# Kernel optimization log

Measured on AMD Instinct MI355X. Metric: run time of the kernel, lower is better.

Reference implementation:

```python
import jax, jax.numpy as jnp
import numpy as np
from jax import lax

# Dimensions
B, D_MODEL, H, W = 2, 128, 96, 96
EXPAND = 2
D_INNER = EXPAND * D_MODEL      # 256
D_STATE = 16
D_CONV = 4
DT_RANK = (D_MODEL + 15) // 16  # 8 (mamba default ceil(d_model/16))


def setup_inputs() -> dict:
    key = jax.random.key(0)
    ks = jax.random.split(key, 16)
    s = 0.02
    return {
        "x": jax.random.normal(ks[0], (B, D_MODEL, H, W), jnp.float32),
        "y": jax.random.normal(ks[1], (B, D_MODEL, H, W), jnp.float32),
        # CrossMambaBlock conv weights (bias=False)
        "w_q": jax.random.normal(ks[2], (D_MODEL, D_MODEL), jnp.float32) * s,
        "w_q_dw": jax.random.normal(ks[3], (D_MODEL, 1, 3, 3), jnp.float32) * s,
        "w_kv": jax.random.normal(ks[4], (2 * D_MODEL, D_MODEL), jnp.float32) * s,
        "w_kv_dw": jax.random.normal(ks[5], (2 * D_MODEL, 1, 3, 3), jnp.float32) * s,
        # Mamba params
        "w_in": jax.random.normal(ks[6], (2 * D_INNER, D_MODEL), jnp.float32) * s,
        "w_conv": jax.random.normal(ks[7], (D_INNER, 1, D_CONV), jnp.float32) * s,
        "b_conv": jnp.zeros((D_INNER,), jnp.float32),
        "w_xproj": jax.random.normal(ks[8], (DT_RANK + 2 * D_STATE, D_INNER), jnp.float32) * s,
        "w_dt": jax.random.normal(ks[9], (D_INNER, DT_RANK), jnp.float32) * s,
        "b_dt": jax.random.normal(ks[10], (D_INNER,), jnp.float32) * s,
        "A_log": jnp.log(jnp.tile(jnp.arange(1, D_STATE + 1, dtype=jnp.float32), (D_INNER, 1))),
        "D_skip": jnp.ones((D_INNER,), jnp.float32),
        "w_out": jax.random.normal(ks[11], (D_MODEL, D_INNER), jnp.float32) * s,
        "w_outproj": jax.random.normal(ks[12], (D_MODEL, D_MODEL), jnp.float32) * s,
    }


def _conv1x1(x, w):
    # 1x1 conv == per-pixel linear over channels
    return jnp.einsum('bchw,oc->bohw', x, w)


def _dw3(x, w):
    # 3x3 depthwise conv, padding 1
    return lax.conv_general_dilated(
        x, w, (1, 1), [(1, 1), (1, 1)],
        dimension_numbers=('NCHW', 'OIHW', 'NCHW'),
        feature_group_count=x.shape[1])


def _mamba(seq, w_in, w_conv, b_conv, w_xproj, w_dt, b_dt, A_log, D_skip, w_out):
    # seq: (b, L, d_model)
    b, L, _ = seq.shape
    xz = seq @ w_in.T                              # (b, L, 2*d_inner)
    xm, z = jnp.split(xz, 2, axis=-1)
    # causal depthwise conv1d along L
    xc = lax.conv_general_dilated(
        xm.transpose(0, 2, 1), w_conv, (1,), [(D_CONV - 1, 0)],
        dimension_numbers=('NCH', 'OIH', 'NCH'),
        feature_group_count=D_INNER)
    xm = jax.nn.silu(xc + b_conv[None, :, None]).transpose(0, 2, 1)  # (b, L, d_inner)
    xdbl = xm @ w_xproj.T                          # (b, L, dt_rank + 2*d_state)
    dt = jax.nn.softplus(xdbl[..., :DT_RANK] @ w_dt.T + b_dt)        # (b, L, d_inner)
    Bm = xdbl[..., DT_RANK:DT_RANK + D_STATE]      # (b, L, n)
    Cm = xdbl[..., DT_RANK + D_STATE:]             # (b, L, n)
    A = -jnp.exp(A_log)                            # (d_inner, n)
    dA = jnp.exp(dt[..., None] * A)                # (b, L, d, n)
    dBu = (dt * xm)[..., None] * Bm[:, :, None, :] # (b, L, d, n)

    def step(h, inp):
        a, bu, c = inp
        h = a * h + bu                             # (b, d, n)
        return h, jnp.einsum('bdn,bn->bd', h, c)

    h0 = jnp.zeros((b, D_INNER, D_STATE), seq.dtype)
    _, ys = lax.scan(step, h0, (dA.transpose(1, 0, 2, 3),
                                dBu.transpose(1, 0, 2, 3),
                                Cm.transpose(1, 0, 2)))
    y = ys.transpose(1, 0, 2) + xm * D_skip        # (b, L, d_inner)
    y = y * jax.nn.silu(z)
    return y @ w_out.T                             # (b, L, d_model)


def reference(x, y, w_q, w_q_dw, w_kv, w_kv_dw, w_in, w_conv, b_conv,
              w_xproj, w_dt, b_dt, A_log, D_skip, w_out, w_outproj):
    b, c, h, w = x.shape
    q = _dw3(_conv1x1(x, w_q), w_q_dw)
    kv = _dw3(_conv1x1(y, w_kv), w_kv_dw)
    k, v = jnp.split(kv, 2, axis=1)
    fused = q + k
    seq = fused.reshape(b, c, h * w).transpose(0, 2, 1)   # b (h w) c
    enh = _mamba(seq, w_in, w_conv, b_conv, w_xproj, w_dt, b_dt,
                 A_log, D_skip, w_out)
    enhanced = enh.transpose(0, 2, 1).reshape(b, c, h, w)
    return _conv1x1(enhanced + v, w_outproj)
```

## Files before the change

### kernel.cpp

```cpp
#include <hip/hip_runtime.h>
#include <hip/hip_bf16.h>
#include <math.h>

#define L_SEQ 9216
#define BATCH 2
#define DM 128
#define DI 256
#define DST 16
#define HH 96
#define WW 96
#define CL 24
#define NC 384
#define P2U 16

typedef __attribute__((ext_vector_type(8))) short short8;
typedef __attribute__((ext_vector_type(4))) float f32x4;

__device__ __forceinline__ unsigned short bf16b(float x) {
    return __builtin_bit_cast(unsigned short, __float2bfloat16(x));
}

__global__ __launch_bounds__(256)
void prep_tr(const float* __restrict__ wq, const float* __restrict__ wkv,
             const float* __restrict__ win, const float* __restrict__ wxp,
             const float* __restrict__ wout, const float* __restrict__ wop,
             unsigned short* __restrict__ qkvh, unsigned short* __restrict__ qkvl,
             unsigned short* __restrict__ winh, unsigned short* __restrict__ winl,
             unsigned short* __restrict__ xph,  unsigned short* __restrict__ xpl,
             unsigned short* __restrict__ wch,  unsigned short* __restrict__ wcl,
             const float* __restrict__ x, const float* __restrict__ y,
             unsigned* __restrict__ xt, unsigned* __restrict__ yt) {
    __shared__ float tile[32][33];
    if (blockIdx.x < 704) {
        int idx = blockIdx.x * 256 + threadIdx.x;
        float v; unsigned short* H; unsigned short* L; int r;
        if (idx < 49152) {
            r = idx; int m = r >> 7, k = r & 127;
            v = (m < 128) ? wq[m * 128 + k] : wkv[(m - 128) * 128 + k];
            H = qkvh; L = qkvl;
        } else if (idx < 114688) {
            r = idx - 49152;
            v = win[r];
            H = winh; L = winl;
        } else if (idx < 131072) {
            r = idx - 114688; int m = r >> 8, k = r & 255;
            v = (m < 40) ? wxp[m * 256 + k] : 0.f;
            H = xph; L = xpl;
        } else if (idx < 180224) {
            r = idx - 131072; int o = r / 384, k = r % 384;
            if (k < 256) {
                float s = 0.f;
                for (int c = 0; c < 128; c++)
                    s = fmaf(wop[o * 128 + c], wout[c * 256 + k], s);
                v = s;
            } else {
                v = wop[o * 128 + (k - 256)];
            }
            H = wch; L = wcl;
        } else return;
        unsigned short hb = bf16b(v);
        float hf = __uint_as_float(((unsigned)hb) << 16);
        H[r] = hb;
        L[r] = bf16b(v - hf);
    } else {
        int id = blockIdx.x - 704;
        int bx = id % 288;
        int rest = id / 288;
        int by = rest & 3;
        int z  = rest >> 2;
        int l0 = bx * 32, c0 = by * 32;
        int b = z & (BATCH - 1);
        const float* src = (z < BATCH) ? x : y;
        unsigned* dst = (z < BATCH) ? xt : yt;
        int tx = threadIdx.x & 31, ty = threadIdx.x >> 5;
#pragma unroll
        for (int j = 0; j < 4; j++)
            tile[ty + 8 * j][tx] = src[((size_t)b * 128 + c0 + ty + 8 * j) * L_SEQ + l0 + tx];
        __syncthreads();
#pragma unroll
        for (int j = 0; j < 4; j++) {
            float v = tile[tx][ty + 8 * j];
            unsigned short hb = bf16b(v);
            float hf = __uint_as_float(((unsigned)hb) << 16);
            unsigned short lb = bf16b(v - hf);
            dst[((size_t)b * L_SEQ + l0 + ty + 8 * j) * 128 + c0 + tx] =
                (((unsigned)hb) << 16) | (unsigned)lb;
        }
    }
}

__global__ __launch_bounds__(256)
void tr_fv(const float* __restrict__ fused, const float* __restrict__ vtmp,
           unsigned* __restrict__ fused_pm, float* __restrict__ yv_pm) {
    __shared__ float tile[32][33];
    int l0 = blockIdx.x * 32, by = blockIdx.y, b = blockIdx.z;
    bool isf = by < 4;
    int c0 = (by & 3) * 32;
    const float* src = isf ? fused : vtmp;
    int tx = threadIdx.x & 31, ty = threadIdx.x >> 5;
#pragma unroll
    for (int j = 0; j < 4; j++)
        tile[ty + 8 * j][tx] = src[((size_t)b * 128 + c0 + ty + 8 * j) * L_SEQ + l0 + tx];
    __syncthreads();
    if (isf) {
#pragma unroll
        for (int j = 0; j < 4; j++) {
            float v = tile[tx][ty + 8 * j];
            unsigned short hb = bf16b(v);
            float hf = __uint_as_float(((unsigned)hb) << 16);
            unsigned short lb = bf16b(v - hf);
            fused_pm[((size_t)b * L_SEQ + l0 + ty + 8 * j) * 128 + c0 + tx] =
                (((unsigned)hb) << 16) | (unsigned)lb;
        }
    } else {
#pragma unroll
        for (int j = 0; j < 4; j++)
            yv_pm[((size_t)b * L_SEQ + l0 + ty + 8 * j) * 384 + 256 + c0 + tx] = tile[tx][ty + 8 * j];
    }
}

template<int K, bool PK>
__launch_bounds__(256)
__global__ void gemm_mfma(const unsigned short* __restrict__ Ah,
                          const unsigned short* __restrict__ Al,
                          const void* __restrict__ BA, const void* __restrict__ BB,
                          int bySplit, int Cb, float* __restrict__ Out, int Mout) {
    __shared__ unsigned short sBh[128 * 40];
    __shared__ unsigned short sBl[128 * 40];
    int t = threadIdx.x;
    int lane = t & 63, w = t >> 6;
    int wm = w >> 1, wn = w & 1;
    int nf = lane & 15, q = lane >> 4;
    int bx = blockIdx.x, by = blockIdx.y, bz = blockIdx.z;
    const void* Bp = (by < bySplit) ? BA : BB;
    const unsigned short* ahp = Ah + (size_t)(by * 64 + wm * 32 + nf) * K + q * 8;
    const unsigned short* alp = Al + (size_t)(by * 64 + wm * 32 + nf) * K + q * 8;

    f32x4 acc[2][4];
#pragma unroll
    for (int i = 0; i < 2; i++)
#pragma unroll
        for (int j = 0; j < 4; j++) acc[i][j] = (f32x4)0.f;

    uint4 gv[4];
    auto gload = [&](int k0) {
#pragma unroll
        for (int i = 0; i < 4; i++) {
            int u = t + i * 256;
            int n = u >> 3, k4 = u & 7;
            if (PK) {
                const unsigned* Bsrc = (const unsigned*)Bp + ((size_t)bz * L_SEQ + bx * 128) * Cb;
                gv[i] = *(const uint4*)(Bsrc + (size_t)n * Cb + k0 + k4 * 4);
            } else {
                const float* Bsrc = (const float*)Bp + ((size_t)bz * L_SEQ + bx * 128) * Cb;
                float4 v = *(const float4*)(Bsrc + (size_t)n * Cb + k0 + k4 * 4);
                gv[i] = *(uint4*)&v;
            }
        }
    };
    auto lwrite = [&]() {
#pragma unroll
        for (int i = 0; i < 4; i++) {
            int u = t + i * 256;
            int n = u >> 3, k4 = u & 7;
            if (PK) {
                uint4 v = gv[i];
                *(unsigned*)&sBh[n * 40 + k4 * 4]     = (v.x >> 16) | (v.y & 0xFFFF0000u);
                *(unsigned*)&sBh[n * 40 + k4 * 4 + 2] = (v.z >> 16) | (v.w & 0xFFFF0000u);
                *(unsigned*)&sBl[n * 40 + k4 * 4]     = (v.x & 0xFFFFu) | (v.y << 16);
                *(unsigned*)&sBl[n * 40 + k4 * 4 + 2] = (v.z & 0xFFFFu) | (v.w << 16);
            } else {
                float4 v = *(float4*)&gv[i];
                unsigned short hx = bf16b(v.x), hy = bf16b(v.y);
                unsigned short hz = bf16b(v.z), hw = bf16b(v.w);
                float fx = __uint_as_float(((unsigned)hx) << 16);
                float fy = __uint_as_float(((unsigned)hy) << 16);
                float fz = __uint_as_float(((unsigned)hz) << 16);
                float fw = __uint_as_float(((unsigned)hw) << 16);
                *(unsigned*)&sBh[n * 40 + k4 * 4]     = (unsigned)hx | (((unsigned)hy) << 16);
                *(unsigned*)&sBh[n * 40 + k4 * 4 + 2] = (unsigned)hz | (((unsigned)hw) << 16);
                *(unsigned*)&sBl[n * 40 + k4 * 4]     = (unsigned)bf16b(v.x - fx) | (((unsigned)bf16b(v.y - fy)) << 16);
                *(unsigned*)&sBl[n * 40 + k4 * 4 + 2] = (unsigned)bf16b(v.z - fz) | (((unsigned)bf16b(v.w - fw)) << 16);
            }
        }
    };

    gload(0);
    short8 a_h[2], a_l[2];
    a_h[0] = *(const short8*)(ahp);
    a_h[1] = *(const short8*)(ahp + 16 * K);
    a_l[0] = *(const short8*)(alp);
    a_l[1] = *(const short8*)(alp + 16 * K);

    for (int k0 = 0; k0 < K; k0 += 32) {
        lwrite();
        __syncthreads();
        bool more = (k0 + 32 < K);
        short8 nh0, nh1, nl0, nl1;
        if (more) {
            gload(k0 + 32);
            nh0 = *(const short8*)(ahp + k0 + 32);
            nh1 = *(const short8*)(ahp + 16 * K + k0 + 32);
            nl0 = *(const short8*)(alp + k0 + 32);
            nl1 = *(const short8*)(alp + 16 * K + k0 + 32);
        }
#pragma unroll
        for (int ns = 0; ns < 4; ns++) {
            int nr = (wn * 64 + ns * 16 + nf) * 40 + q * 8;
            short8 bh = *(const short8*)&sBh[nr];
            short8 bl = *(const short8*)&sBl[nr];
#pragma unroll
            for (int ms = 0; ms < 2; ms++) {
                acc[ms][ns] = __builtin_amdgcn_mfma_f32_16x16x32_bf16(a_h[ms], bh, acc[ms][ns], 0, 0, 0);
                acc[ms][ns] = __builtin_amdgcn_mfma_f32_16x16x32_bf16(a_h[ms], bl, acc[ms][ns], 0, 0, 0);
                acc[ms][ns] = __builtin_amdgcn_mfma_f32_16x16x32_bf16(a_l[ms], bh, acc[ms][ns], 0, 0, 0);
            }
        }
        __syncthreads();
        if (more) { a_h[0] = nh0; a_h[1] = nh1; a_l[0] = nl0; a_l[1] = nl1; }
    }
#pragma unroll
    for (int ms = 0; ms < 2; ms++)
#pragma unroll
        for (int ns = 0; ns < 4; ns++) {
            int o0 = by * 64 + wm * 32 + ms * 16 + q * 4;
            int col = bx * 128 + wn * 64 + ns * 16 + nf;
            size_t base = (size_t)bz * Mout * L_SEQ + (size_t)o0 * L_SEQ + col;
#pragma unroll
            for (int i = 0; i < 4; i++)
                Out[base + (size_t)i * L_SEQ] = acc[ms][ns][i];
        }
}

__launch_bounds__(256)
__global__ void gemm_xz_conv(const unsigned short* __restrict__ Ah,
                             const unsigned short* __restrict__ Al,
                             const unsigned* __restrict__ Bpk,
                             const float* __restrict__ w_conv,
                             const float* __restrict__ b_conv,
                             float* __restrict__ xm_pm, float* __restrict__ z_pm) {
    constexpr int K = 128;
    __shared__ __align__(16) char smem[131 * 68 * 4];
    unsigned short* sBh = (unsigned short*)smem;
    unsigned short* sBl = sBh + 128 * 40;
    float (*sxz)[68] = (float (*)[68])smem;
    int t = threadIdx.x;
    int lane = t & 63, w = t >> 6;
    int wm = w >> 1, wn = w & 1;
    int nf = lane & 15, q = lane >> 4;
    int bx = blockIdx.x, by = blockIdx.y, bz = blockIdx.z;
    const unsigned short* ahp = Ah + (size_t)(by * 64 + wm * 32 + nf) * K + q * 8;
    const unsigned short* alp = Al + (size_t)(by * 64 + wm * 32 + nf) * K + q * 8;

    f32x4 acc[2][4];
#pragma unroll
    for (int i = 0; i < 2; i++)
#pragma unroll
        for (int j = 0; j < 4; j++) acc[i][j] = (f32x4)0.f;

    uint4 gv[4];
    auto gload = [&](int k0) {
#pragma unroll
        for (int i = 0; i < 4; i++) {
            int u = t + i * 256;
            int n = u >> 3, k4 = u & 7;
            const unsigned* Bsrc = Bpk + ((size_t)bz * L_SEQ + bx * 128) * K;
            gv[i] = *(const uint4*)(Bsrc + (size_t)n * K + k0 + k4 * 4);
        }
    };
    auto lwrite = [&]() {
#pragma unroll
        for (int i = 0; i < 4; i++) {
            int u = t + i * 256;
            int n = u >> 3, k4 = u & 7;
            uint4 v = gv[i];
            *(unsigned*)&sBh[n * 40 + k4 * 4]     = (v.x >> 16) | (v.y & 0xFFFF0000u);
            *(unsigned*)&sBh[n * 40 + k4 * 4 + 2] = (v.z >> 16) | (v.w & 0xFFFF0000u);
            *(unsigned*)&sBl[n * 40 + k4 * 4]     = (v.x & 0xFFFFu) | (v.y << 16);
            *(unsigned*)&sBl[n * 40 + k4 * 4 + 2] = (v.z & 0xFFFFu) | (v.w << 16);
        }
    };

    gload(0);
    short8 a_h[2], a_l[2];
    a_h[0] = *(const short8*)(ahp);
    a_h[1] = *(const short8*)(ahp + 16 * K);
    a_l[0] = *(const short8*)(alp);
    a_l[1] = *(const short8*)(alp + 16 * K);

    for (int k0 = 0; k0 < K; k0 += 32) {
        lwrite();
        __syncthreads();
        bool more = (k0 + 32 < K);
        short8 nh0, nh1, nl0, nl1;
        if (more) {
            gload(k0 + 32);
            nh0 = *(const short8*)(ahp + k0 + 32);
            nh1 = *(const short8*)(ahp + 16 * K + k0 + 32);
            nl0 = *(const short8*)(alp + k0 + 32);
            nl1 = *(const short8*)(alp + 16 * K + k0 + 32);
        }
#pragma unroll
        for (int ns = 0; ns < 4; ns++) {
            int nr = (wn * 64 + ns * 16 + nf) * 40 + q * 8;
            short8 bh = *(const short8*)&sBh[nr];
            short8 bl = *(const short8*)&sBl[nr];
#pragma unroll
            for (int ms = 0; ms < 2; ms++) {
                acc[ms][ns] = __builtin_amdgcn_mfma_f32_16x16x32_bf16(a_h[ms], bh, acc[ms][ns], 0, 0, 0);
                acc[ms][ns] = __builtin_amdgcn_mfma_f32_16x16x32_bf16(a_h[ms], bl, acc[ms][ns], 0, 0, 0);
                acc[ms][ns] = __builtin_amdgcn_mfma_f32_16x16x32_bf16(a_l[ms], bh, acc[ms][ns], 0, 0, 0);
            }
        }
        __syncthreads();
        if (more) { a_h[0] = nh0; a_h[1] = nh1; a_l[0] = nl0; a_l[1] = nl1; }
    }

    bool isxm = by < 4;
    if (isxm && t < 192) {
        int hi = t >> 6, dloc = t & 63;
        int lp = bx * 128 - 3 + hi;
        float s = 0.f;
        if (lp >= 0) {
            const unsigned* bp = Bpk + ((size_t)bz * L_SEQ + lp) * K;
            const unsigned short* ar_h = Ah + (size_t)(by * 64 + dloc) * K;
            const unsigned short* ar_l = Al + (size_t)(by * 64 + dloc) * K;
            for (int k = 0; k < K; k++) {
                unsigned bw = bp[k];
                float bh = __uint_as_float(bw & 0xFFFF0000u);
                float bl = __uint_as_float(bw << 16);
                float ah = __uint_as_float(((unsigned)ar_h[k]) << 16);
                float al = __uint_as_float(((unsigned)ar_l[k]) << 16);
                s = fmaf(ah, bh, s);
                s = fmaf(ah, bl, s);
                s = fmaf(al, bh, s);
            }
        }
        sxz[hi][dloc] = s;
    }
#pragma unroll
    for (int ms = 0; ms < 2; ms++)
#pragma unroll
        for (int ns = 0; ns < 4; ns++) {
            int l = wn * 64 + ns * 16 + nf;
            int dl = wm * 32 + ms * 16 + q * 4;
            *(float4*)&sxz[3 + l][dl] = *(float4*)&acc[ms][ns];
        }
    __syncthreads();

    int dloc = t & 63;
    int lsub = t >> 6;
    int dglob = (by & 3) * 64 + dloc;
    if (isxm) {
        float4 wc = *(const float4*)&w_conv[dglob * 4];
        float bc = b_conv[dglob];
        float* outp = xm_pm + ((size_t)bz * L_SEQ + bx * 128) * DI + dglob;
#pragma unroll
        for (int it = 0; it < 32; it++) {
            int l = it * 4 + lsub;
            float xc = sxz[l][dloc] * wc.x + sxz[l + 1][dloc] * wc.y
                     + sxz[l + 2][dloc] * wc.z + sxz[l + 3][dloc] * wc.w + bc;
            outp[(size_t)l * DI] = xc / (1.f + __expf(-xc));
        }
    } else {
        float* outp = z_pm + ((size_t)bz * L_SEQ + bx * 128) * DI + dglob;
#pragma unroll
        for (int it = 0; it < 32; it++) {
            int l = it * 4 + lsub;
            float z = sxz[3 + l][dloc];
            outp[(size_t)l * DI] = z / (1.f + __expf(-z));
        }
    }
}

__global__ __launch_bounds__(256)
void dw3_fuse(const float* __restrict__ qkv0,
              const float* __restrict__ wq_dw, const float* __restrict__ wkv_dw,
              float* __restrict__ fused, float* __restrict__ vtmp) {
    __shared__ float sk[34][100];
    __shared__ float sq[34][100];
    int vt = blockIdx.x;
    int c  = blockIdx.y;
    int b  = blockIdx.z;
    int h0 = vt * 32;
    int t = threadIdx.x;
    bool two = (c < DM);
    const float* pk = qkv0 + ((size_t)b * 384 + 128 + c) * L_SEQ;
    const float* pq = qkv0 + ((size_t)b * 384 + c) * L_SEQ;
    for (int idx = t; idx < 34 * 98; idx += 256) {
        int r = idx / 98, col = idx % 98;
        int h = h0 - 1 + r, w = col - 1;
        bool ok = (h >= 0 && h < HH && w >= 0 && w < WW);
        sk[r][col] = ok ? pk[h * WW + w] : 0.f;
        if (two) sq[r][col] = ok ? pq[h * WW + w] : 0.f;
    }
    float k9k[9], k9q[9];
#pragma unroll
    for (int i = 0; i < 9; i++) k9k[i] = wkv_dw[c * 9 + i];
    if (two)
#pragma unroll
        for (int i = 0; i < 9; i++) k9q[i] = wq_dw[c * 9 + i];
    __syncthreads();

    int row = t >> 3, col0 = (t & 7) * 12;
    float rk[3][14];
#pragma unroll
    for (int dr = 0; dr < 3; dr++)
#pragma unroll
        for (int cc = 0; cc < 14; cc++) rk[dr][cc] = sk[row + dr][col0 + cc];
    float outv[12];
#pragma unroll
    for (int j = 0; j < 12; j++) {
        float s = 0.f;
#pragma unroll
        for (int dr = 0; dr < 3; dr++)
#pragma unroll
            for (int dc = 0; dc < 3; dc++)
                s = fmaf(rk[dr][j + dc], k9k[dr * 3 + dc], s);
        outv[j] = s;
    }
    if (two) {
        float rq[3][14];
#pragma unroll
        for (int dr = 0; dr < 3; dr++)
#pragma unroll
            for (int cc = 0; cc < 14; cc++) rq[dr][cc] = sq[row + dr][col0 + cc];
#pragma unroll
        for (int j = 0; j < 12; j++) {
            float s = outv[j];
#pragma unroll
            for (int dr = 0; dr < 3; dr++)
#pragma unroll
                for (int dc = 0; dc < 3; dc++)
                    s = fmaf(rq[dr][j + dc], k9q[dr * 3 + dc], s);
            outv[j] = s;
        }
    }
    float* dst = (two ? fused + ((size_t)b * DM + c) * L_SEQ
                      : vtmp + ((size_t)b * DM + (c - DM)) * L_SEQ)
               + (h0 + row) * WW + col0;
#pragma unroll
    for (int j = 0; j < 12; j++) dst[j] = outv[j];
}

__global__ __launch_bounds__(256)
void scan_p1(const float* __restrict__ xm_pm, const float* __restrict__ xdbl,
             const float* __restrict__ w_dt, const float* __restrict__ b_dt,
             float* __restrict__ Sbuf, float* __restrict__ rPbuf) {
    __shared__ float sB[CL][DST + 1];
    __shared__ float sDt[CL][9];
    int blk = blockIdx.x;
    int b = blk / NC, ch = blk % NC;
    int l0 = ch * CL;
    int d = threadIdx.x;
    for (int idx = threadIdx.x; idx < CL * DST; idx += 256) {
        int n = idx / CL, lc = idx % CL;
        sB[lc][n] = xdbl[((size_t)b * 64 + 8 + n) * L_SEQ + l0 + lc];
    }
    for (int idx = threadIdx.x; idx < CL * 8; idx += 256) {
        int r = idx / CL, lc = idx % CL;
        sDt[lc][r] = xdbl[((size_t)b * 64 + r) * L_SEQ + l0 + lc];
    }
    float wdt[8];
    *(float4*)&wdt[0] = *(const float4*)&w_dt[d * 8];
    *(float4*)&wdt[4] = *(const float4*)&w_dt[d * 8 + 4];
    float bdt = b_dt[d];
    float h[DST];
#pragma unroll
    for (int n = 0; n < DST; n++) h[n] = 0.f;
    float rP = 1.f;
    __syncthreads();
    const float* xmp = xm_pm + ((size_t)b * L_SEQ + l0) * DI + d;
    float xmv = xmp[0];
    for (int lc = 0; lc < CL; lc++) {
        float xmn = (lc + 1 < CL) ? xmp[(size_t)(lc + 1) * DI] : 0.f;
        float s = bdt;
#pragma unroll
        for (int r = 0; r < 8; r++) s = fmaf(wdt[r], sDt[lc][r], s);
        float e = __expf(s);
        float rr = __builtin_amdgcn_rcpf(1.f + e);
        float dtv = -__logf(rr);
        float dx = dtv * xmv;
        float a = 1.f;
#pragma unroll
        for (int n = 0; n < DST; n++) {
            a *= rr;
            h[n] = fmaf(a, h[n], dx * sB[lc][n]);
        }
        rP *= rr;
        xmv = xmn;
    }
    float* sp = Sbuf + (size_t)blk * DST * DI + d;
#pragma unroll
    for (int n = 0; n < DST; n++) sp[(size_t)n * DI] = h[n];
    rPbuf[(size_t)blk * DI + d] = rP;
}

__global__ __launch_bounds__(256)
void scan_p2(const float* __restrict__ rPbuf, const float* __restrict__ Sbuf,
             float* __restrict__ Hinit) {
    int bn = blockIdx.x;
    int b = bn >> 4, n = bn & 15;
    int d = threadIdx.x;
    int n1 = n + 1;
    const float* rp = rPbuf + (size_t)b * NC * DI + d;
    const float* sp = Sbuf + ((size_t)b * NC * DST + n) * DI + d;
    float* hp = Hinit + ((size_t)b * NC * DST + n) * DI + d;
    const size_t strS = (size_t)DST * DI;
    float h = 0.f;
    float r[P2U], s[P2U];
#pragma unroll
    for (int i = 0; i < P2U; i++) {
        r[i] = rp[(size_t)i * DI];
        s[i] = sp[(size_t)i * strS];
    }
    for (int c = 0; c < NC; c += P2U) {
        float rn[P2U], sn[P2U];
        bool more = (c + P2U < NC);
        if (more) {
#pragma unroll
            for (int i = 0; i < P2U; i++) {
                rn[i] = rp[(size_t)(c + P2U + i) * DI];
                sn[i] = sp[(size_t)(c + P2U + i) * strS];
            }
        }
#pragma unroll
        for (int i = 0; i < P2U; i++) {
            hp[(size_t)(c + i) * strS] = h;
            float rr = r[i];
            float r2 = rr * rr, r4 = r2 * r2, r8 = r4 * r4;
            float a = 1.f;
            if (n1 & 1) a *= rr;
            if (n1 & 2) a *= r2;
            if (n1 & 4) a *= r4;
            if (n1 & 8) a *= r8;
            if (n1 & 16) a = r8 * r8;
            h = fmaf(a, h, s[i]);
        }
        if (more) {
#pragma unroll
            for (int i = 0; i < P2U; i++) { r[i] = rn[i]; s[i] = sn[i]; }
        }
    }
}

__global__ __launch_bounds__(256)
void scan_p3(const float* __restrict__ xm_pm, const float* __restrict__ xdbl,
             const float* __restrict__ w_dt, const float* __restrict__ b_dt,
             const float* __restrict__ Hinit, const float* __restrict__ Dskip,
             const float* __restrict__ z_pm, float* __restrict__ yv_pm) {
    __shared__ float sB[CL][DST + 1];
    __shared__ float sC[CL][DST + 1];
    __shared__ float sDt[CL][9];
    int blk = blockIdx.x;
    int b = blk / NC, ch = blk % NC;
    int l0 = ch * CL;
    int d = threadIdx.x;
    for (int idx = threadIdx.x; idx < CL * DST; idx += 256) {
        int n = idx / CL, lc = idx % CL;
        sB[lc][n] = xdbl[((size_t)b * 64 + 8 + n) * L_SEQ + l0 + lc];
        sC[lc][n] = xdbl[((size_t)b * 64 + 24 + n) * L_SEQ + l0 + lc];
    }
    for (int idx = threadIdx.x; idx < CL * 8; idx += 256) {
        int r = idx / CL, lc = idx % CL;
        sDt[lc][r] = xdbl[((size_t)b * 64 + r) * L_SEQ + l0 + lc];
    }
    float wdt[8];
    *(float4*)&wdt[0] = *(const float4*)&w_dt[d * 8];
    *(float4*)&wdt[4] = *(const float4*)&w_dt[d * 8 + 4];
    float bdt = b_dt[d];
    float h[DST];
    const float* hi = Hinit + (size_t)blk * DST * DI + d;
#pragma unroll
    for (int n = 0; n < DST; n++) h[n] = hi[(size_t)n * DI];
    float dsk = Dskip[d];
    __syncthreads();
    const float* xmp = xm_pm + ((size_t)b * L_SEQ + l0) * DI + d;
    const float* zp  = z_pm + ((size_t)b * L_SEQ + l0) * DI + d;
    float* yp = yv_pm + ((size_t)b * L_SEQ + l0) * 384 + d;
    float xmv = xmp[0];
    float zv  = zp[0];
    for (int lc = 0; lc < CL; lc++) {
        float xmn = 0.f, zn = 0.f;
        if (lc + 1 < CL) {
            xmn = xmp[(size_t)(lc + 1) * DI];
            zn  = zp[(size_t)(lc + 1) * DI];
        }
        float s = bdt;
#pragma unroll
        for (int r = 0; r < 8; r++) s = fmaf(wdt[r], sDt[lc][r], s);
        float e = __expf(s);
        float rr = __builtin_amdgcn_rcpf(1.f + e);
        float dtv = -__logf(rr);
        float dx = dtv * xmv;
        float a = 1.f;
        float yvv = 0.f;
#pragma unroll
        for (int n = 0; n < DST; n++) {
            a *= rr;
            h[n] = fmaf(a, h[n], dx * sB[lc][n]);
            yvv = fmaf(h[n], sC[lc][n], yvv);
        }
        yvv = fmaf(xmv, dsk, yvv);
        yp[(size_t)lc * 384] = yvv * zv;
        xmv = xmn; zv = zn;
    }
}

extern "C" void kernel_launch(void* const* d_in, const int* in_sizes, int n_in,
                              void* d_out, int out_size, void* d_ws, size_t ws_size,
                              hipStream_t stream) {
    const float* x        = (const float*)d_in[0];
    const float* y        = (const float*)d_in[1];
    const float* w_q      = (const float*)d_in[2];
    const float* w_q_dw   = (const float*)d_in[3];
    const float* w_kv     = (const float*)d_in[4];
    const float* w_kv_dw  = (const float*)d_in[5];
    const float* w_in     = (const float*)d_in[6];
    const float* w_conv   = (const float*)d_in[7];
    const float* b_conv   = (const float*)d_in[8];
    const float* w_xproj  = (const float*)d_in[9];
    const float* w_dt     = (const float*)d_in[10];
    const float* b_dt     = (const float*)d_in[11];
    const float* D_skip   = (const float*)d_in[13];
    const float* w_out    = (const float*)d_in[14];
    const float* w_outproj= (const float*)d_in[15];
    float* out = (float*)d_out;
    (void)in_sizes; (void)n_in; (void)out_size; (void)ws_size;

    char* base = (char*)d_ws;
    size_t off = 0;
    auto allocB = [&](size_t bytes) { void* p = base + off; off += (bytes + 255) & ~(size_t)255; return p; };
    const size_t PL = (size_t)BATCH * DM * L_SEQ;
    float*    qkv0    = (float*)allocB(3 * PL * 4);
    float*    fused   = (float*)allocB(PL * 4);
    unsigned* xt      = (unsigned*)allocB(PL * 4);
    unsigned* yt      = (unsigned*)allocB(PL * 4);
    float*    yv_pm   = (float*)allocB(3 * PL * 4);
    float*    xm_pm   = (float*)allocB(2 * PL * 4);
    float*    z_pm    = (float*)allocB(2 * PL * 4);
    float*    xdbl    = (float*)allocB(PL * 2);
    const size_t SC = (size_t)BATCH * NC * DI * DST;
    float* Sb  = (float*)allocB(SC * 4);
    float* Hb  = (float*)allocB(SC * 4);
    float* rPb = (float*)allocB((size_t)BATCH * NC * DI * 4);
    unsigned short* qkvh = (unsigned short*)allocB(49152 * 2);
    unsigned short* qkvl = (unsigned short*)allocB(49152 * 2);
    unsigned short* winh = (unsigned short*)allocB(65536 * 2);
    unsigned short* winl = (unsigned short*)allocB(65536 * 2);
    unsigned short* xph  = (unsigned short*)allocB(16384 * 2);
    unsigned short* xpl  = (unsigned short*)allocB(16384 * 2);
    unsigned short* wch  = (unsigned short*)allocB(49152 * 2);
    unsigned short* wcl  = (unsigned short*)allocB(49152 * 2);
    unsigned* fused_pm = xt;
    float*    vtmp     = (float*)yt;

    prep_tr<<<704 + 4608, 256, 0, stream>>>(w_q, w_kv, w_in, w_xproj, w_out, w_outproj,
                                            qkvh, qkvl, winh, winl, xph, xpl, wch, wcl,
                                            x, y, xt, yt);

    gemm_mfma<128, true><<<dim3(72, 6, BATCH), 256, 0, stream>>>(
        qkvh, qkvl, xt, yt, 2, 128, qkv0, 384);

    dw3_fuse<<<dim3(3, 256, BATCH), 256, 0, stream>>>(qkv0, w_q_dw, w_kv_dw, fused, vtmp);

    tr_fv<<<dim3(288, 8, BATCH), 256, 0, stream>>>(fused, vtmp, fused_pm, yv_pm);

    gemm_xz_conv<<<dim3(72, 8, BATCH), 256, 0, stream>>>(
        winh, winl, fused_pm, w_conv, b_conv, xm_pm, z_pm);

    gemm_mfma<256, false><<<dim3(72, 1, BATCH), 256, 0, stream>>>(
        xph, xpl, xm_pm, xm_pm, 1, 256, xdbl, 64);

    scan_p1<<<BATCH * NC, 256, 0, stream>>>(xm_pm, xdbl, w_dt, b_dt, Sb, rPb);
    scan_p2<<<32, 256, 0, stream>>>(rPb, Sb, Hb);
    scan_p3<<<BATCH * NC, 256, 0, stream>>>(xm_pm, xdbl, w_dt, b_dt, Hb, D_skip, z_pm, yv_pm);

    gemm_mfma<384, false><<<dim3(72, 2, BATCH), 256, 0, stream>>>(
        wch, wcl, yv_pm, yv_pm, 2, 384, out, 128);
}
```

Before: 268.4 us.

## Shrink LDS in xz GEMM epilogue and write z directly from registers

Cuts the gemm_xz_conv shared-memory footprint from a 131x68 float staging tile to the B-operand buffer size. The epilogue now runs in two passes of 32 channels, with the three halo rows kept in a separate small array. The z-half blocks apply SiLU in registers and store float4s straight to global memory, skipping the LDS round trip and the barrier. The halo dot product is vectorized with 16-byte loads and split accumulators. A min-blocks launch bound is added to raise occupancy, at the cost of an extra barrier in the xm path and possible register pressure.

After: 260.2 us, median of 3. 3.1% less time.

```diff
diff --git a/kernel.cpp b/kernel.cpp
--- a/kernel.cpp
+++ b/kernel.cpp
@@ -232,7 +232,7 @@
         }
 }
 
-__launch_bounds__(256)
+__launch_bounds__(256, 4)
 __global__ void gemm_xz_conv(const unsigned short* __restrict__ Ah,
                              const unsigned short* __restrict__ Al,
                              const unsigned* __restrict__ Bpk,
@@ -240,10 +240,11 @@
                              const float* __restrict__ b_conv,
                              float* __restrict__ xm_pm, float* __restrict__ z_pm) {
     constexpr int K = 128;
-    __shared__ __align__(16) char smem[131 * 68 * 4];
+    __shared__ __align__(16) char smem[128 * 40 * 2 * 2];
+    __shared__ float shalo[3][64];
     unsigned short* sBh = (unsigned short*)smem;
     unsigned short* sBl = sBh + 128 * 40;
-    float (*sxz)[68] = (float (*)[68])smem;
+    float (*sxz)[36] = (float (*)[36])smem;
     int t = threadIdx.x;
     int lane = t & 63, w = t >> 6;
     int wm = w >> 1, wn = w & 1;
@@ -317,58 +318,83 @@
     }
 
     bool isxm = by < 4;
-    if (isxm && t < 192) {
+    if (!isxm) {
+#pragma unroll
+        for (int ms = 0; ms < 2; ms++)
+#pragma unroll
+            for (int ns = 0; ns < 4; ns++) {
+                int l = wn * 64 + ns * 16 + nf;
+                int d0 = wm * 32 + ms * 16 + q * 4;
+                float4 v;
+                float a0 = acc[ms][ns][0], a1 = acc[ms][ns][1];
+                float a2 = acc[ms][ns][2], a3 = acc[ms][ns][3];
+                v.x = a0 / (1.f + __expf(-a0));
+                v.y = a1 / (1.f + __expf(-a1));
+                v.z = a2 / (1.f + __expf(-a2));
+                v.w = a3 / (1.f + __expf(-a3));
+                *(float4*)&z_pm[((size_t)bz * L_SEQ + bx * 128 + l) * DI + (by & 3) * 64 + d0] = v;
+            }
+        return;
+    }
+
+    if (t < 192) {
         int hi = t >> 6, dloc = t & 63;
         int lp = bx * 128 - 3 + hi;
-        float s = 0.f;
+        float s0 = 0.f, s1 = 0.f;
         if (lp >= 0) {
-            const unsigned* bp = Bpk + ((size_t)bz * L_SEQ + lp) * K;
-            const unsigned short* ar_h = Ah + (size_t)(by * 64 + dloc) * K;
-            const unsigned short* ar_l = Al + (size_t)(by * 64 + dloc) * K;
-            for (int k = 0; k < K; k++) {
-                unsigned bw = bp[k];
-                float bh = __uint_as_float(bw & 0xFFFF0000u);
-                float bl = __uint_as_float(bw << 16);
-                float ah = __uint_as_float(((unsigned)ar_h[k]) << 16);
-                float al = __uint_as_float(((unsigned)ar_l[k]) << 16);
-                s = fmaf(ah, bh, s);
-                s = fmaf(ah, bl, s);
-                s = fmaf(al, bh, s);
-            }
-        }
-        sxz[hi][dloc] = s;
-    }
-#pragma unroll
-    for (int ms = 0; ms < 2; ms++)
-#pragma unroll
-        for (int ns = 0; ns < 4; ns++) {
-            int l = wn * 64 + ns * 16 + nf;
-            int dl = wm * 32 + ms * 16 + q * 4;
-            *(float4*)&sxz[3 + l][dl] = *(float4*)&acc[ms][ns];
-        }
-    __syncthreads();
-
-    int dloc = t & 63;
-    int lsub = t >> 6;
-    int dglob = (by & 3) * 64 + dloc;
-    if (isxm) {
+            const uint4* bp4 = (const uint4*)(Bpk + ((size_t)bz * L_SEQ + lp) * K);
+            const short8* ah8 = (const short8*)(Ah + (size_t)(by * 64 + dloc) * K);
+            const short8* al8 = (const short8*)(Al + (size_t)(by * 64 + dloc) * K);
+#pragma unroll 4
+            for (int k8 = 0; k8 < 16; k8++) {
+                uint4 b0 = bp4[2 * k8], b1 = bp4[2 * k8 + 1];
+                short8 ah = ah8[k8], al = al8[k8];
+                unsigned bw[8] = {b0.x, b0.y, b0.z, b0.w, b1.x, b1.y, b1.z, b1.w};
+#pragma unroll
+                for (int j = 0; j < 8; j++) {
+                    float bh = __uint_as_float(bw[j] & 0xFFFF0000u);
+                    float bl = __uint_as_float(bw[j] << 16);
+                    float vh = __uint_as_float(((unsigned)(ah[j] & 0xFFFF)) << 16);
+                    float vl = __uint_as_float(((unsigned)(al[j] & 0xFFFF)) << 16);
+                    s0 = fmaf(vh, bh, s0);
+                    s1 = fmaf(vh, bl, s1);
+                    s0 = fmaf(vl, bh, s0);
+                }
+            }
+        }
+        shalo[hi][dloc] = s0 + s1;
+    }
+
+    int dl = t & 31;
+    int lr = t >> 5;
+#pragma unroll
+    for (int p = 0; p < 2; p++) {
+        if (p == 1) __syncthreads();
+        if (wm == p) {
+#pragma unroll
+            for (int ms = 0; ms < 2; ms++)
+#pragma unroll
+                for (int ns = 0; ns < 4; ns++) {
+                    int l = wn * 64 + ns * 16 + nf;
+                    *(float4*)&sxz[l][ms * 16 + q * 4] = *(float4*)&acc[ms][ns];
+                }
+        }
+        __syncthreads();
+        int dglob = by * 64 + p * 32 + dl;
         float4 wc = *(const float4*)&w_conv[dglob * 4];
         float bc = b_conv[dglob];
         float* outp = xm_pm + ((size_t)bz * L_SEQ + bx * 128) * DI + dglob;
 #pragma unroll
-        for (int it = 0; it < 32; it++) {
-            int l = it * 4 + lsub;
-            float xc = sxz[l][dloc] * wc.x + sxz[l + 1][dloc] * wc.y
-                     + sxz[l + 2][dloc] * wc.z + sxz[l + 3][dloc] * wc.w + bc;
+        for (int it = 0; it < 16; it++) {
+            int l = it * 8 + lr;
+            float xv[4];
+#pragma unroll
+            for (int dd = 0; dd < 4; dd++) {
+                int j = l - 3 + dd;
+                xv[dd] = (j >= 0) ? sxz[j][dl] : shalo[j + 3][p * 32 + dl];
+            }
+            float xc = xv[0] * wc.x + xv[1] * wc.y + xv[2] * wc.z + xv[3] * wc.w + bc;
             outp[(size_t)l * DI] = xc / (1.f + __expf(-xc));
-        }
-    } else {
-        float* outp = z_pm + ((size_t)bz * L_SEQ + bx * 128) * DI + dglob;
-#pragma unroll
-        for (int it = 0; it < 32; it++) {
-            int l = it * 4 + lsub;
-            float z = sxz[3 + l][dloc];
-            outp[(size_t)l * DI] = z / (1.f + __expf(-z));
         }
     }
 }
```
